# Kernel optimization log

Measured on AMD Instinct MI355X. Metric: run time of the kernel, lower is better.

## Reference

```python
import jax, jax.numpy as jnp
import numpy as np

B, S, F, H, O = 256, 512, 64, 1024, 24  # batch, seq_len, input_size, hidden_size, output_size


def setup_inputs() -> dict:
    key = jax.random.key(0)
    ks = jax.random.split(key, 11)
    s = 1.0 / np.sqrt(H)  # PyTorch LSTM/Linear uniform init bound
    u = lambda k, shape: jax.random.uniform(k, shape, jnp.float32, -s, s)
    return {
        "x": jax.random.normal(ks[0], (B, S, F), jnp.float32),
        # layer 0 (gate order: i, f, g, o stacked along first dim)
        "W_ih0": u(ks[1], (4 * H, F)),
        "W_hh0": u(ks[2], (4 * H, H)),
        "b_ih0": u(ks[3], (4 * H,)),
        "b_hh0": u(ks[4], (4 * H,)),
        # layer 1
        "W_ih1": u(ks[5], (4 * H, H)),
        "W_hh1": u(ks[6], (4 * H, H)),
        "b_ih1": u(ks[7], (4 * H,)),
        "b_hh1": u(ks[8], (4 * H,)),
        # final projection over all timesteps: [O, H*S]
        "fc_W": jax.random.uniform(ks[9], (O, H * S), jnp.float32, -1.0 / np.sqrt(H * S), 1.0 / np.sqrt(H * S)),
        "fc_b": jax.random.uniform(ks[10], (O,), jnp.float32, -1.0 / np.sqrt(H * S), 1.0 / np.sqrt(H * S)),
    }


def _lstm_layer(x_sbf, W_ih, W_hh, b_ih, b_hh):
    # x_sbf: [S, B, Fin]; returns all hidden states [S, B, H]
    Hh = W_hh.shape[1]
    # precompute input contribution for all steps (one big GEMM)
    xg = jnp.einsum('sbf,gf->sbg', x_sbf, W_ih) + b_ih + b_hh  # [S, B, 4H]

    def step(carry, xg_t):
        h, c = carry
        gates = xg_t + h @ W_hh.T  # [B, 4H]
        i, f, g, o = jnp.split(gates, 4, axis=-1)
        c = jax.nn.sigmoid(f) * c + jax.nn.sigmoid(i) * jnp.tanh(g)
        h = jax.nn.sigmoid(o) * jnp.tanh(c)
        return (h, c), h

    h0 = jnp.zeros((x_sbf.shape[1], Hh), x_sbf.dtype)
    _, hs = jax.lax.scan(step, (h0, h0), xg)
    return hs  # [S, B, H]


def reference(x, W_ih0, W_hh0, b_ih0, b_hh0, W_ih1, W_hh1, b_ih1, b_hh1, fc_W, fc_b):
    xs = jnp.swapaxes(x, 0, 1)  # [S, B, F]
    h1 = _lstm_layer(xs, W_ih0, W_hh0, b_ih0, b_hh0)  # [S, B, H]
    h2 = _lstm_layer(h1, W_ih1, W_hh1, b_ih1, b_hh1)  # [S, B, H]
    # use_all_h=True: reshape [B, S, H] -> [B, S*H], then Linear
    flat = jnp.swapaxes(h2, 0, 1).reshape(x.shape[0], -1)
    return flat @ fc_W.T + fc_b  # [B, O]
```

## Files before the change

kernel.cpp:

```cpp
#include <hip/hip_runtime.h>
#include <hip/hip_fp16.h>

#define B_ 256
#define S_ 512
#define F_ 64
#define H_ 1024
#define O_ 24
#define G_ 4096

typedef _Float16 half_t;
typedef _Float16 h8 __attribute__((ext_vector_type(8)));
typedef float f4 __attribute__((ext_vector_type(4)));

#define OFF_H1 ((size_t)0)
#define OFF_H2 (OFF_H1 + (size_t)2*B_*H_*2)
#define OFF_C1 (OFF_H2 + (size_t)2*B_*H_*2)
#define OFF_C2 (OFF_C1 + (size_t)B_*H_*4)
#define OFF_OP (OFF_C2 + (size_t)B_*H_*4)
#define ZBYTES (OFF_OP + (size_t)32*B_*O_*4)
#define OFF_BIAS0 (ZBYTES)
#define OFF_BIAS1 (OFF_BIAS0 + (size_t)G_*4)
#define OFF_XH    (OFF_BIAS1 + (size_t)G_*4)
#define OFF_WIH0  (OFF_XH + (size_t)B_*S_*F_*2)
#define OFF_WHH0  (OFF_WIH0 + (size_t)G_*F_*2)
#define OFF_WIH1  (OFF_WHH0 + (size_t)G_*H_*2)
#define OFF_WHH1  (OFF_WIH1 + (size_t)G_*H_*2)
#define WS_NEEDED (OFF_WHH1 + (size_t)G_*H_*2)

__global__ void k_bias(const float* __restrict__ bi0, const float* __restrict__ bh0,
                       const float* __restrict__ bi1, const float* __restrict__ bh1,
                       float* __restrict__ bias0, float* __restrict__ bias1) {
    int i = blockIdx.x * blockDim.x + threadIdx.x;
    if (i < G_) { bias0[i] = bi0[i] + bh0[i]; bias1[i] = bi1[i] + bh1[i]; }
}

__global__ void k_cvt(const float* __restrict__ src, half_t* __restrict__ dst, int n) {
    int i = blockIdx.x * blockDim.x + threadIdx.x;
    int stride = gridDim.x * blockDim.x;
    for (; i < n; i += stride) dst[i] = (half_t)src[i];
}

__global__ void k_pack(const float* __restrict__ src, half_t* __restrict__ dst, int NC) {
    int i = blockIdx.x * blockDim.x + threadIdx.x;
    int total = 32768 * NC;
    if (i >= total) return;
    int lane = i & 63;
    int j    = (i >> 6) & 3;
    int ck   = (i >> 8) % NC;
    int gh   = i / (256 * NC);
    int srow = (gh >> 5) * H_ + (gh & 31) * 32 + (j >> 1) * 16 + (lane & 15);
    int scol = ck * 64 + (j & 1) * 32 + (lane >> 4) * 8;
    const float* s = src + (size_t)srow * (NC * 64) + scol;
    h8 v;
    #pragma unroll
    for (int e = 0; e < 8; ++e) v[e] = (half_t)s[e];
    *(h8*)&dst[(size_t)i * 8] = v;
}

__global__ __launch_bounds__(256, 2)
void k_phase(int t,
             const half_t* __restrict__ x_h,
             const half_t* __restrict__ Wih0, const half_t* __restrict__ Whh0,
             const float* __restrict__ bias0, float* __restrict__ c1, half_t* __restrict__ h1buf,
             const half_t* __restrict__ Wih1, const half_t* __restrict__ Whh1,
             const float* __restrict__ bias1, float* __restrict__ c2, half_t* __restrict__ h2buf,
             const float* __restrict__ fcW, float* __restrict__ out_part)
{
    __shared__ __align__(16) char smraw[23040];
    half_t* A_s    = (half_t*)smraw;
    float*  gate_s = (float*)smraw;
    float*  h_s    = (float*)(smraw + 4 * 32 * 33 * 4);

    const int n  = blockIdx.x;
    const bool l1 = (n < 256);
    const int m  = l1 ? n : n - 256;
    const int ht = (m & 7) + 8 * ((m >> 3) & 3);
    const int bt = (m >> 5) & 7;

    int tt; const half_t* xb; int ldx, cx; const half_t* Wih;
    const half_t* Whh; const float* bias; float* c; half_t* hn_out; const half_t* hp;
    if (l1) {
        if (t == 0) return;
        tt = t - 1;
        xb  = h1buf + (size_t)(tt & 1) * B_ * H_;  ldx = H_;      cx = 16;
        Wih = Wih1;  Whh = Whh1;  bias = bias1;  c = c2;
        hp     = h2buf + (size_t)((tt - 1) & 1) * B_ * H_;
        hn_out = h2buf + (size_t)(tt & 1) * B_ * H_;
    } else {
        if (t >= S_) return;
        tt = t;
        xb  = x_h + (size_t)tt * F_;  ldx = S_ * F_;  cx = 1;
        Wih = Wih0;  Whh = Whh0;  bias = bias0;  c = c1;
        hp     = h1buf + (size_t)((tt - 1) & 1) * B_ * H_;
        hn_out = h1buf + (size_t)(tt & 1) * B_ * H_;
    }

    const int thr  = threadIdx.x;
    const int wave = thr >> 6, lane = thr & 63;
    const int quad = lane >> 4, l15 = lane & 15;
    const int hbase = ht * 32;

    float bv0 = bias[wave * H_ + hbase + l15];
    float bv1 = bias[wave * H_ + hbase + 16 + l15];
    f4 acc[2][2];
    #pragma unroll
    for (int mt = 0; mt < 2; ++mt) {
        acc[mt][0] = (f4){bv0, bv0, bv0, bv0};
        acc[mt][1] = (f4){bv1, bv1, bv1, bv1};
    }

    const int nchunks = cx + 16;
    const int ar = thr >> 3;
    const int ak = (thr & 7) * 8;

    const int ghW = wave * 32 + ht;

    f4 pA;
    h8 c0, c1r, c2r, c3;
    h8 n0, n1, n2, n3;

    auto fetchA = [&](int ck) {
        const half_t* Ab; int lda, k0;
        if (ck < cx) { Ab = xb; lda = ldx; k0 = ck * 64; }
        else         { Ab = hp; lda = H_;  k0 = (ck - cx) * 64; }
        pA = *(const f4*)&Ab[(size_t)(bt * 32 + ar) * lda + k0 + ak];
    };
    auto fetchW = [&](int ck, h8& r0, h8& r1, h8& r2, h8& r3) {
        const half_t* Wb; int ckk, NC;
        if (ck < cx) { Wb = Wih; ckk = ck;      NC = cx; }
        else         { Wb = Whh; ckk = ck - cx; NC = 16; }
        const half_t* base = Wb + ((size_t)(((ghW * NC) + ckk) * 4) * 64 + lane) * 8;
        r0 = *(const h8*)(base + 0 * 512);
        r1 = *(const h8*)(base + 1 * 512);
        r2 = *(const h8*)(base + 2 * 512);
        r3 = *(const h8*)(base + 3 * 512);
    };

    fetchA(0);
    fetchW(0, c0, c1r, c2r, c3);
    for (int ck = 0; ck < nchunks; ++ck) {
        *(f4*)&A_s[ar * 72 + ak] = pA;
        __syncthreads();
        if (ck + 1 < nchunks) { fetchA(ck + 1); fetchW(ck + 1, n0, n1, n2, n3); }

        h8 a0 = *(const h8*)&A_s[(0  + l15) * 72 + 0 + quad * 8];
        h8 a1 = *(const h8*)&A_s[(16 + l15) * 72 + 0 + quad * 8];
        acc[0][0] = __builtin_amdgcn_mfma_f32_16x16x32_f16(a0, c0,  acc[0][0], 0, 0, 0);
        acc[0][1] = __builtin_amdgcn_mfma_f32_16x16x32_f16(a0, c2r, acc[0][1], 0, 0, 0);
        acc[1][0] = __builtin_amdgcn_mfma_f32_16x16x32_f16(a1, c0,  acc[1][0], 0, 0, 0);
        acc[1][1] = __builtin_amdgcn_mfma_f32_16x16x32_f16(a1, c2r, acc[1][1], 0, 0, 0);
        h8 a2 = *(const h8*)&A_s[(0  + l15) * 72 + 32 + quad * 8];
        h8 a3 = *(const h8*)&A_s[(16 + l15) * 72 + 32 + quad * 8];
        acc[0][0] = __builtin_amdgcn_mfma_f32_16x16x32_f16(a2, c1r, acc[0][0], 0, 0, 0);
        acc[0][1] = __builtin_amdgcn_mfma_f32_16x16x32_f16(a2, c3,  acc[0][1], 0, 0, 0);
        acc[1][0] = __builtin_amdgcn_mfma_f32_16x16x32_f16(a3, c1r, acc[1][0], 0, 0, 0);
        acc[1][1] = __builtin_amdgcn_mfma_f32_16x16x32_f16(a3, c3,  acc[1][1], 0, 0, 0);
        __syncthreads();

        c0 = n0; c1r = n1; c2r = n2; c3 = n3;
    }

    #pragma unroll
    for (int mt = 0; mt < 2; ++mt)
        #pragma unroll
        for (int nt = 0; nt < 2; ++nt)
            #pragma unroll
            for (int r = 0; r < 4; ++r)
                gate_s[wave * (32 * 33) + (mt * 16 + quad * 4 + r) * 33 + nt * 16 + l15] = acc[mt][nt][r];
    __syncthreads();

    #pragma unroll
    for (int kk = 0; kk < 4; ++kk) {
        int e = thr + kk * 256;
        int b = e >> 5, col = e & 31;
        float gi = gate_s[0 * (32 * 33) + b * 33 + col];
        float gf = gate_s[1 * (32 * 33) + b * 33 + col];
        float gg = gate_s[2 * (32 * 33) + b * 33 + col];
        float go = gate_s[3 * (32 * 33) + b * 33 + col];
        float si = 1.f / (1.f + __expf(-gi));
        float sf = 1.f / (1.f + __expf(-gf));
        float so = 1.f / (1.f + __expf(-go));
        float tg = tanhf(gg);
        size_t cidx = (size_t)(bt * 32 + b) * H_ + hbase + col;
        float cn = sf * c[cidx] + si * tg;
        c[cidx] = cn;
        float hnv = so * tanhf(cn);
        hn_out[cidx] = (half_t)hnv;
        h_s[b * 33 + col] = hnv;
    }

    if (l1) {
        __syncthreads();
        const float* fcWt = fcW + (size_t)tt * H_;
        for (int p = thr; p < 32 * O_; p += 256) {
            int o = p >> 5, bb = p & 31;
            float s = 0.f;
            #pragma unroll 8
            for (int j = 0; j < 32; ++j)
                s += h_s[bb * 33 + j] * fcWt[(size_t)o * (S_ * H_) + hbase + j];
            out_part[ht * (B_ * O_) + (bt * 32 + bb) * O_ + o] += s;
        }
    }
}

__global__ void k_final(const float* __restrict__ out_part, const float* __restrict__ fcb,
                        float* __restrict__ out) {
    int i = blockIdx.x * blockDim.x + threadIdx.x;
    if (i >= B_ * O_) return;
    int o = i % O_;
    float s = fcb[o];
    for (int t = 0; t < 32; ++t) s += out_part[t * (B_ * O_) + i];
    out[i] = s;
}

extern "C" void kernel_launch(void* const* d_in, const int* in_sizes, int n_in,
                              void* d_out, int out_size, void* d_ws, size_t ws_size,
                              hipStream_t stream) {
    const float* x    = (const float*)d_in[0];
    const float* Wih0 = (const float*)d_in[1];
    const float* Whh0 = (const float*)d_in[2];
    const float* bih0 = (const float*)d_in[3];
    const float* bhh0 = (const float*)d_in[4];
    const float* Wih1 = (const float*)d_in[5];
    const float* Whh1 = (const float*)d_in[6];
    const float* bih1 = (const float*)d_in[7];
    const float* bhh1 = (const float*)d_in[8];
    const float* fcW  = (const float*)d_in[9];
    const float* fcb  = (const float*)d_in[10];

    char* ws = (char*)d_ws;
    half_t* h1buf  = (half_t*)(ws + OFF_H1);
    half_t* h2buf  = (half_t*)(ws + OFF_H2);
    float*  c1     = (float*)(ws + OFF_C1);
    float*  c2     = (float*)(ws + OFF_C2);
    float*  opart  = (float*)(ws + OFF_OP);
    float*  bias0  = (float*)(ws + OFF_BIAS0);
    float*  bias1  = (float*)(ws + OFF_BIAS1);
    half_t* x_h    = (half_t*)(ws + OFF_XH);
    half_t* wih0_p = (half_t*)(ws + OFF_WIH0);
    half_t* whh0_p = (half_t*)(ws + OFF_WHH0);
    half_t* wih1_p = (half_t*)(ws + OFF_WIH1);
    half_t* whh1_p = (half_t*)(ws + OFF_WHH1);

    hipMemsetAsync(d_ws, 0, ZBYTES, stream);

    k_bias<<<dim3((G_ + 255) / 256), dim3(256), 0, stream>>>(bih0, bhh0, bih1, bhh1, bias0, bias1);
    k_cvt<<<dim3(2048), dim3(256), 0, stream>>>(x, x_h, B_ * S_ * F_);
    k_pack<<<dim3(128),  dim3(256), 0, stream>>>(Wih0, wih0_p, 1);
    k_pack<<<dim3(2048), dim3(256), 0, stream>>>(Whh0, whh0_p, 16);
    k_pack<<<dim3(2048), dim3(256), 0, stream>>>(Wih1, wih1_p, 16);
    k_pack<<<dim3(2048), dim3(256), 0, stream>>>(Whh1, whh1_p, 16);

    dim3 grid(512), blk(256);
    for (int t = 0; t <= S_; ++t) {
        k_phase<<<grid, blk, 0, stream>>>(t, x_h,
                                          wih0_p, whh0_p, bias0, c1, h1buf,
                                          wih1_p, whh1_p, bias1, c2, h2buf,
                                          fcW, opart);
    }
    k_final<<<dim3((B_ * O_ + 255) / 256), dim3(256), 0, stream>>>(opart, fcb, (float*)d_out);
}
```

Baseline: 11.57 ms.

## Load A operands directly into registers, drop LDS staging and per-chunk barriers

```diff
diff --git a/kernel.cpp b/kernel.cpp
--- a/kernel.cpp
+++ b/kernel.cpp
@@ -66,10 +66,8 @@
              const float* __restrict__ bias1, float* __restrict__ c2, half_t* __restrict__ h2buf,
              const float* __restrict__ fcW, float* __restrict__ out_part)
 {
-    __shared__ __align__(16) char smraw[23040];
-    half_t* A_s    = (half_t*)smraw;
-    float*  gate_s = (float*)smraw;
-    float*  h_s    = (float*)(smraw + 4 * 32 * 33 * 4);
+    __shared__ float gate_s[4][32 * 33];
+    __shared__ float h_s[32 * 33];
 
     const int n  = blockIdx.x;
     const bool l1 = (n < 256);
@@ -110,55 +108,64 @@
     }
 
     const int nchunks = cx + 16;
-    const int ar = thr >> 3;
-    const int ak = (thr & 7) * 8;
-
     const int ghW = wave * 32 + ht;
 
-    f4 pA;
-    h8 c0, c1r, c2r, c3;
-    h8 n0, n1, n2, n3;
-
-    auto fetchA = [&](int ck) {
+    const int arow0 = bt * 32 + l15;
+    const int arow1 = arow0 + 16;
+    const int akq   = quad * 8;
+
+    auto fetchA = [&](int ck, h8& a0, h8& a1, h8& a2, h8& a3) {
         const half_t* Ab; int lda, k0;
         if (ck < cx) { Ab = xb; lda = ldx; k0 = ck * 64; }
         else         { Ab = hp; lda = H_;  k0 = (ck - cx) * 64; }
-        pA = *(const f4*)&Ab[(size_t)(bt * 32 + ar) * lda + k0 + ak];
+        const half_t* r0 = Ab + (size_t)arow0 * lda + k0 + akq;
+        const half_t* r1 = Ab + (size_t)arow1 * lda + k0 + akq;
+        a0 = *(const h8*)(r0);
+        a1 = *(const h8*)(r1);
+        a2 = *(const h8*)(r0 + 32);
+        a3 = *(const h8*)(r1 + 32);
     };
-    auto fetchW = [&](int ck, h8& r0, h8& r1, h8& r2, h8& r3) {
+    auto fetchW = [&](int ck, h8& w0, h8& w1, h8& w2, h8& w3) {
         const half_t* Wb; int ckk, NC;
         if (ck < cx) { Wb = Wih; ckk = ck;      NC = cx; }
         else         { Wb = Whh; ckk = ck - cx; NC = 16; }
         const half_t* base = Wb + ((size_t)(((ghW * NC) + ckk) * 4) * 64 + lane) * 8;
-        r0 = *(const h8*)(base + 0 * 512);
-        r1 = *(const h8*)(base + 1 * 512);
-        r2 = *(const h8*)(base + 2 * 512);
-        r3 = *(const h8*)(base + 3 * 512);
+        w0 = *(const h8*)(base + 0 * 512);
+        w1 = *(const h8*)(base + 1 * 512);
+        w2 = *(const h8*)(base + 2 * 512);
+        w3 = *(const h8*)(base + 3 * 512);
     };
 
-    fetchA(0);
-    fetchW(0, c0, c1r, c2r, c3);
-    for (int ck = 0; ck < nchunks; ++ck) {
-        *(f4*)&A_s[ar * 72 + ak] = pA;
-        __syncthreads();
-        if (ck + 1 < nchunks) { fetchA(ck + 1); fetchW(ck + 1, n0, n1, n2, n3); }
-
-        h8 a0 = *(const h8*)&A_s[(0  + l15) * 72 + 0 + quad * 8];
-        h8 a1 = *(const h8*)&A_s[(16 + l15) * 72 + 0 + quad * 8];
-        acc[0][0] = __builtin_amdgcn_mfma_f32_16x16x32_f16(a0, c0,  acc[0][0], 0, 0, 0);
-        acc[0][1] = __builtin_amdgcn_mfma_f32_16x16x32_f16(a0, c2r, acc[0][1], 0, 0, 0);
-        acc[1][0] = __builtin_amdgcn_mfma_f32_16x16x32_f16(a1, c0,  acc[1][0], 0, 0, 0);
-        acc[1][1] = __builtin_amdgcn_mfma_f32_16x16x32_f16(a1, c2r, acc[1][1], 0, 0, 0);
-        h8 a2 = *(const h8*)&A_s[(0  + l15) * 72 + 32 + quad * 8];
-        h8 a3 = *(const h8*)&A_s[(16 + l15) * 72 + 32 + quad * 8];
-        acc[0][0] = __builtin_amdgcn_mfma_f32_16x16x32_f16(a2, c1r, acc[0][0], 0, 0, 0);
-        acc[0][1] = __builtin_amdgcn_mfma_f32_16x16x32_f16(a2, c3,  acc[0][1], 0, 0, 0);
-        acc[1][0] = __builtin_amdgcn_mfma_f32_16x16x32_f16(a3, c1r, acc[1][0], 0, 0, 0);
-        acc[1][1] = __builtin_amdgcn_mfma_f32_16x16x32_f16(a3, c3,  acc[1][1], 0, 0, 0);
-        __syncthreads();
-
-        c0 = n0; c1r = n1; c2r = n2; c3 = n3;
-    }
+    h8 xa0, xa1, xa2, xa3, xw0, xw1, xw2, xw3;
+    h8 ya0, ya1, ya2, ya3, yw0, yw1, yw2, yw3;
+
+    #define MFMA_SET(a0v,a1v,a2v,a3v,w0v,w1v,w2v,w3v)                                  \
+        acc[0][0] = __builtin_amdgcn_mfma_f32_16x16x32_f16(a0v, w0v, acc[0][0], 0,0,0);\
+        acc[0][1] = __builtin_amdgcn_mfma_f32_16x16x32_f16(a0v, w2v, acc[0][1], 0,0,0);\
+        acc[1][0] = __builtin_amdgcn_mfma_f32_16x16x32_f16(a1v, w0v, acc[1][0], 0,0,0);\
+        acc[1][1] = __builtin_amdgcn_mfma_f32_16x16x32_f16(a1v, w2v, acc[1][1], 0,0,0);\
+        acc[0][0] = __builtin_amdgcn_mfma_f32_16x16x32_f16(a2v, w1v, acc[0][0], 0,0,0);\
+        acc[0][1] = __builtin_amdgcn_mfma_f32_16x16x32_f16(a2v, w3v, acc[0][1], 0,0,0);\
+        acc[1][0] = __builtin_amdgcn_mfma_f32_16x16x32_f16(a3v, w1v, acc[1][0], 0,0,0);\
+        acc[1][1] = __builtin_amdgcn_mfma_f32_16x16x32_f16(a3v, w3v, acc[1][1], 0,0,0);
+
+    fetchA(0, xa0, xa1, xa2, xa3);
+    fetchW(0, xw0, xw1, xw2, xw3);
+    const int npair = nchunks >> 1;
+    for (int p = 0; p < npair; ++p) {
+        const int k0 = 2 * p;
+        fetchA(k0 + 1, ya0, ya1, ya2, ya3);
+        fetchW(k0 + 1, yw0, yw1, yw2, yw3);
+        MFMA_SET(xa0, xa1, xa2, xa3, xw0, xw1, xw2, xw3)
+        const int k2 = (k0 + 2 == nchunks) ? k0 + 1 : k0 + 2;
+        fetchA(k2, xa0, xa1, xa2, xa3);
+        fetchW(k2, xw0, xw1, xw2, xw3);
+        MFMA_SET(ya0, ya1, ya2, ya3, yw0, yw1, yw2, yw3)
+    }
+    if (nchunks & 1) {
+        MFMA_SET(xa0, xa1, xa2, xa3, xw0, xw1, xw2, xw3)
+    }
+    #undef MFMA_SET
 
     #pragma unroll
     for (int mt = 0; mt < 2; ++mt)
@@ -166,17 +173,17 @@
         for (int nt = 0; nt < 2; ++nt)
             #pragma unroll
             for (int r = 0; r < 4; ++r)
-                gate_s[wave * (32 * 33) + (mt * 16 + quad * 4 + r) * 33 + nt * 16 + l15] = acc[mt][nt][r];
+                gate_s[wave][(mt * 16 + quad * 4 + r) * 33 + nt * 16 + l15] = acc[mt][nt][r];
     __syncthreads();
 
     #pragma unroll
     for (int kk = 0; kk < 4; ++kk) {
         int e = thr + kk * 256;
         int b = e >> 5, col = e & 31;
-        float gi = gate_s[0 * (32 * 33) + b * 33 + col];
-        float gf = gate_s[1 * (32 * 33) + b * 33 + col];
-        float gg = gate_s[2 * (32 * 33) + b * 33 + col];
-        float go = gate_s[3 * (32 * 33) + b * 33 + col];
+        float gi = gate_s[0][b * 33 + col];
+        float gf = gate_s[1][b * 33 + col];
+        float gg = gate_s[2][b * 33 + col];
+        float go = gate_s[3][b * 33 + col];
         float si = 1.f / (1.f + __expf(-gi));
         float sf = 1.f / (1.f + __expf(-gf));
         float so = 1.f / (1.f + __expf(-go));
```

Result: slower. 17.50 ms (+51.3%).

## Stage eight A chunks per barrier pair and double-buffer weight registers

Applied to the files above, without the earlier changes.

```diff
diff --git a/kernel.cpp b/kernel.cpp
--- a/kernel.cpp
+++ b/kernel.cpp
@@ -61,15 +61,15 @@
 void k_phase(int t,
              const half_t* __restrict__ x_h,
              const half_t* __restrict__ Wih0, const half_t* __restrict__ Whh0,
-             const float* __restrict__ bias0, float* __restrict__ c1, half_t* __restrict__ h1buf,
+             const float* __restrict__ bias0, float* __restrict__ c1g, half_t* __restrict__ h1buf,
              const half_t* __restrict__ Wih1, const half_t* __restrict__ Whh1,
-             const float* __restrict__ bias1, float* __restrict__ c2, half_t* __restrict__ h2buf,
+             const float* __restrict__ bias1, float* __restrict__ c2g, half_t* __restrict__ h2buf,
              const float* __restrict__ fcW, float* __restrict__ out_part)
 {
-    __shared__ __align__(16) char smraw[23040];
+    __shared__ __align__(16) char smraw[36864];
     half_t* A_s    = (half_t*)smraw;
     float*  gate_s = (float*)smraw;
-    float*  h_s    = (float*)(smraw + 4 * 32 * 33 * 4);
+    float*  h_s    = (float*)(smraw + 16896);
 
     const int n  = blockIdx.x;
     const bool l1 = (n < 256);
@@ -83,14 +83,14 @@
         if (t == 0) return;
         tt = t - 1;
         xb  = h1buf + (size_t)(tt & 1) * B_ * H_;  ldx = H_;      cx = 16;
-        Wih = Wih1;  Whh = Whh1;  bias = bias1;  c = c2;
+        Wih = Wih1;  Whh = Whh1;  bias = bias1;  c = c2g;
         hp     = h2buf + (size_t)((tt - 1) & 1) * B_ * H_;
         hn_out = h2buf + (size_t)(tt & 1) * B_ * H_;
     } else {
         if (t >= S_) return;
         tt = t;
         xb  = x_h + (size_t)tt * F_;  ldx = S_ * F_;  cx = 1;
-        Wih = Wih0;  Whh = Whh0;  bias = bias0;  c = c1;
+        Wih = Wih0;  Whh = Whh0;  bias = bias0;  c = c1g;
         hp     = h1buf + (size_t)((tt - 1) & 1) * B_ * H_;
         hn_out = h1buf + (size_t)(tt & 1) * B_ * H_;
     }
@@ -110,20 +110,15 @@
     }
 
     const int nchunks = cx + 16;
-    const int ar = thr >> 3;
-    const int ak = (thr & 7) * 8;
-
     const int ghW = wave * 32 + ht;
-
-    f4 pA;
-    h8 c0, c1r, c2r, c3;
-    h8 n0, n1, n2, n3;
-
-    auto fetchA = [&](int ck) {
+    const int ar  = thr >> 3;
+    const int ak  = (thr & 7) * 8;
+
+    auto loadA = [&](int ck) -> f4 {
         const half_t* Ab; int lda, k0;
         if (ck < cx) { Ab = xb; lda = ldx; k0 = ck * 64; }
         else         { Ab = hp; lda = H_;  k0 = (ck - cx) * 64; }
-        pA = *(const f4*)&Ab[(size_t)(bt * 32 + ar) * lda + k0 + ak];
+        return *(const f4*)&Ab[(size_t)(bt * 32 + ar) * lda + k0 + ak];
     };
     auto fetchW = [&](int ck, h8& r0, h8& r1, h8& r2, h8& r3) {
         const half_t* Wb; int ckk, NC;
@@ -136,29 +131,60 @@
         r3 = *(const h8*)(base + 3 * 512);
     };
 
-    fetchA(0);
-    fetchW(0, c0, c1r, c2r, c3);
-    for (int ck = 0; ck < nchunks; ++ck) {
-        *(f4*)&A_s[ar * 72 + ak] = pA;
+    for (int s = 0; s < nchunks; s += 8) {
+        const int ns = (nchunks - s < 8) ? (nchunks - s) : 8;
+
+        f4 p0, p1, p2, p3, p4, p5, p6, p7;
+              p0 = loadA(s + 0);
+        if (ns > 1)     p1 = loadA(s + 1);
+        if (ns > 2)     p2 = loadA(s + 2);
+        if (ns > 3)     p3 = loadA(s + 3);
+        if (ns > 4)     p4 = loadA(s + 4);
+        if (ns > 5)     p5 = loadA(s + 5);
+        if (ns > 6)     p6 = loadA(s + 6);
+        if (ns > 7)     p7 = loadA(s + 7);
         __syncthreads();
-        if (ck + 1 < nchunks) { fetchA(ck + 1); fetchW(ck + 1, n0, n1, n2, n3); }
-
-        h8 a0 = *(const h8*)&A_s[(0  + l15) * 72 + 0 + quad * 8];
-        h8 a1 = *(const h8*)&A_s[(16 + l15) * 72 + 0 + quad * 8];
-        acc[0][0] = __builtin_amdgcn_mfma_f32_16x16x32_f16(a0, c0,  acc[0][0], 0, 0, 0);
-        acc[0][1] = __builtin_amdgcn_mfma_f32_16x16x32_f16(a0, c2r, acc[0][1], 0, 0, 0);
-        acc[1][0] = __builtin_amdgcn_mfma_f32_16x16x32_f16(a1, c0,  acc[1][0], 0, 0, 0);
-        acc[1][1] = __builtin_amdgcn_mfma_f32_16x16x32_f16(a1, c2r, acc[1][1], 0, 0, 0);
-        h8 a2 = *(const h8*)&A_s[(0  + l15) * 72 + 32 + quad * 8];
-        h8 a3 = *(const h8*)&A_s[(16 + l15) * 72 + 32 + quad * 8];
-        acc[0][0] = __builtin_amdgcn_mfma_f32_16x16x32_f16(a2, c1r, acc[0][0], 0, 0, 0);
-        acc[0][1] = __builtin_amdgcn_mfma_f32_16x16x32_f16(a2, c3,  acc[0][1], 0, 0, 0);
-        acc[1][0] = __builtin_amdgcn_mfma_f32_16x16x32_f16(a3, c1r, acc[1][0], 0, 0, 0);
-        acc[1][1] = __builtin_amdgcn_mfma_f32_16x16x32_f16(a3, c3,  acc[1][1], 0, 0, 0);
+              *(f4*)&A_s[0 * 2304 + ar * 72 + ak] = p0;
+        if (ns > 1)     *(f4*)&A_s[1 * 2304 + ar * 72 + ak] = p1;
+        if (ns > 2)     *(f4*)&A_s[2 * 2304 + ar * 72 + ak] = p2;
+        if (ns > 3)     *(f4*)&A_s[3 * 2304 + ar * 72 + ak] = p3;
+        if (ns > 4)     *(f4*)&A_s[4 * 2304 + ar * 72 + ak] = p4;
+        if (ns > 5)     *(f4*)&A_s[5 * 2304 + ar * 72 + ak] = p5;
+        if (ns > 6)     *(f4*)&A_s[6 * 2304 + ar * 72 + ak] = p6;
+        if (ns > 7)     *(f4*)&A_s[7 * 2304 + ar * 72 + ak] = p7;
         __syncthreads();
 
-        c0 = n0; c1r = n1; c2r = n2; c3 = n3;
-    }
+        h8 xw0, xw1, xw2, xw3, yw0, yw1, yw2, yw3;
+        fetchW(s, xw0, xw1, xw2, xw3);
+
+        #define STEP(i, C0,C1,C2,C3, N0,N1,N2,N3)                                              \
+        if (i < ns) {                                                                          \
+            if (i + 1 < ns) fetchW(s + i + 1, N0, N1, N2, N3);                                 \
+            h8 a0 = *(const h8*)&A_s[i * 2304 + (0  + l15) * 72 + 0  + quad * 8];              \
+            h8 a1 = *(const h8*)&A_s[i * 2304 + (16 + l15) * 72 + 0  + quad * 8];              \
+            h8 a2 = *(const h8*)&A_s[i * 2304 + (0  + l15) * 72 + 32 + quad * 8];              \
+            h8 a3 = *(const h8*)&A_s[i * 2304 + (16 + l15) * 72 + 32 + quad * 8];              \
+            acc[0][0] = __builtin_amdgcn_mfma_f32_16x16x32_f16(a0, C0, acc[0][0], 0,0,0);      \
+            acc[0][1] = __builtin_amdgcn_mfma_f32_16x16x32_f16(a0, C2, acc[0][1], 0,0,0);      \
+            acc[1][0] = __builtin_amdgcn_mfma_f32_16x16x32_f16(a1, C0, acc[1][0], 0,0,0);      \
+            acc[1][1] = __builtin_amdgcn_mfma_f32_16x16x32_f16(a1, C2, acc[1][1], 0,0,0);      \
+            acc[0][0] = __builtin_amdgcn_mfma_f32_16x16x32_f16(a2, C1, acc[0][0], 0,0,0);      \
+            acc[0][1] = __builtin_amdgcn_mfma_f32_16x16x32_f16(a2, C3, acc[0][1], 0,0,0);      \
+            acc[1][0] = __builtin_amdgcn_mfma_f32_16x16x32_f16(a3, C1, acc[1][0], 0,0,0);      \
+            acc[1][1] = __builtin_amdgcn_mfma_f32_16x16x32_f16(a3, C3, acc[1][1], 0,0,0);      \
+        }
+        STEP(0, xw0,xw1,xw2,xw3, yw0,yw1,yw2,yw3)
+        STEP(1, yw0,yw1,yw2,yw3, xw0,xw1,xw2,xw3)
+        STEP(2, xw0,xw1,xw2,xw3, yw0,yw1,yw2,yw3)
+        STEP(3, yw0,yw1,yw2,yw3, xw0,xw1,xw2,xw3)
+        STEP(4, xw0,xw1,xw2,xw3, yw0,yw1,yw2,yw3)
+        STEP(5, yw0,yw1,yw2,yw3, xw0,xw1,xw2,xw3)
+        STEP(6, xw0,xw1,xw2,xw3, yw0,yw1,yw2,yw3)
+        STEP(7, yw0,yw1,yw2,yw3, xw0,xw1,xw2,xw3)
+        #undef STEP
+    }
+
+    __syncthreads();
 
     #pragma unroll
     for (int mt = 0; mt < 2; ++mt)
@@ -194,11 +220,11 @@
         const float* fcWt = fcW + (size_t)tt * H_;
         for (int p = thr; p < 32 * O_; p += 256) {
             int o = p >> 5, bb = p & 31;
-            float s = 0.f;
+            float s2 = 0.f;
             #pragma unroll 8
             for (int j = 0; j < 32; ++j)
-                s += h_s[bb * 33 + j] * fcWt[(size_t)o * (S_ * H_) + hbase + j];
-            out_part[ht * (B_ * O_) + (bt * 32 + bb) * O_ + o] += s;
+                s2 += h_s[bb * 33 + j] * fcWt[(size_t)o * (S_ * H_) + hbase + j];
+            out_part[ht * (B_ * O_) + (bt * 32 + bb) * O_ + o] += s2;
         }
     }
 }
```

Result: faster. 10.52 ms (-9.1%).
